# Performance work log

Hardware: AMD Instinct MI355X
Metric: run time of the kernel (lower is better)

## Reference

```python
import jax, jax.numpy as jnp
import numpy as np
import math

EPS = 1e-08
KERNEL = 3
PAD = KERNEL // 2


def setup_inputs() -> dict:
    key = jax.random.key(0)
    k1, k2, k3, k4 = jax.random.split(key, 4)
    B, C_in, C_out, H, W, S = 8, 512, 512, 64, 64, 512
    x = jax.random.normal(k1, (B, C_in, H, W), dtype=jnp.float32)
    style = jax.random.normal(k2, (B, S), dtype=jnp.float32)
    # modulation Linear: kaiming_normal fan_in linear => std = 1/sqrt(S); bias filled with 1
    w_mod = jax.random.normal(k3, (C_in, S), dtype=jnp.float32) / math.sqrt(S)
    b_mod = jnp.ones((C_in,), dtype=jnp.float32)
    # conv weight: randn / sqrt(in * k^2)
    weight = jax.random.normal(k4, (1, C_out, C_in, KERNEL, KERNEL), dtype=jnp.float32) / math.sqrt(C_in * KERNEL * KERNEL)
    return {"x": x, "style": style, "w_mod": w_mod, "b_mod": b_mod, "weight": weight}


def _modconv(x, style, w_mod, b_mod, weight):
    # style modulation: (B, S) @ (S, C_in) + bias -> (B, 1, C_in, 1, 1)
    s = style @ w_mod.T + b_mod
    w = weight * s[:, None, :, None, None]            # (B, C_out, C_in, k, k)
    # demodulate: rsqrt of sum of squares over (in, kh, kw)
    demod = jax.lax.rsqrt(jnp.sum(w * w, axis=(2, 3, 4)) + EPS)  # (B, C_out)
    w = w * demod[:, :, None, None, None]

    # groups=B conv == per-sample conv; vmap over batch
    def conv1(xb, wb):
        # xb: (C_in, H, W), wb: (C_out, C_in, k, k)
        return jax.lax.conv_general_dilated(
            xb[None], wb, window_strides=(1, 1),
            padding=[(PAD, PAD), (PAD, PAD)],
            dimension_numbers=("NCHW", "OIHW", "NCHW"))[0]

    return jax.vmap(conv1)(x, w)  # (B, C_out, H, W)


def reference(x, style, w_mod, b_mod, weight):
    return _modconv(x, style, w_mod, b_mod, weight)
```

## Files before the change

### kernel.cpp

```cpp
#include <hip/hip_runtime.h>
#include <hip/hip_bf16.h>

#define BATCH 8
#define CIN   512
#define COUT  512
#define HH    64
#define WW    64
#define SS    512
#define HP    66
#define WP    66
#define NPIX  (HH*WW)

typedef __bf16 bfrag  __attribute__((ext_vector_type(8)));
typedef float  f32x4  __attribute__((ext_vector_type(4)));
typedef unsigned short u16x8 __attribute__((ext_vector_type(8)));

__device__ __forceinline__ void async_copy16(const __hip_bfloat16* g, __hip_bfloat16* l) {
    __builtin_amdgcn_global_load_lds(
        (const __attribute__((address_space(1))) void*)g,
        (__attribute__((address_space(3))) void*)l,
        16, 0, 0);
}

__device__ __forceinline__ bool is_f32(const void* b_mod) {
    return ((const unsigned int*)b_mod)[0] == 0x3F800000u;
}

__global__ void k_prep(const void* __restrict__ style,
                       const void* __restrict__ w_mod,
                       const void* __restrict__ b_mod,
                       const void* __restrict__ weight,
                       float* __restrict__ s_out,
                       float* __restrict__ wsq,
                       __hip_bfloat16* __restrict__ Wt) {
    const bool f32 = is_f32(b_mod);
    if (blockIdx.x < 1024) {
        int tid = blockIdx.x * 256 + threadIdx.x;
        float sq = 0.f;
        if (f32) {
            const float* w = (const float*)weight + (size_t)tid * 9;
#pragma unroll
            for (int k = 0; k < 9; ++k) {
                float v = w[k];
                sq += v * v;
                Wt[k * (COUT * CIN) + tid] = __float2bfloat16(v);
            }
        } else {
            const __hip_bfloat16* w = (const __hip_bfloat16*)weight + (size_t)tid * 9;
#pragma unroll
            for (int k = 0; k < 9; ++k) {
                float v = __bfloat162float(w[k]);
                sq += v * v;
                Wt[k * (COUT * CIN) + tid] = w[k];
            }
        }
        wsq[tid] = sq;
    } else {
        int gw   = (blockIdx.x - 1024) * 4 + (threadIdx.x >> 6);
        int lane = threadIdx.x & 63;
        int b = gw >> 9, i = gw & 511;
        int base = lane * 8;
        float acc = 0.f;
        if (f32) {
            const float* st = (const float*)style + b * SS + base;
            const float* wm = (const float*)w_mod + i * SS + base;
#pragma unroll
            for (int j = 0; j < 8; ++j) acc += st[j] * wm[j];
        } else {
            const __hip_bfloat16* st = (const __hip_bfloat16*)style + b * SS + base;
            const __hip_bfloat16* wm = (const __hip_bfloat16*)w_mod + i * SS + base;
#pragma unroll
            for (int j = 0; j < 8; ++j)
                acc += __bfloat162float(st[j]) * __bfloat162float(wm[j]);
        }
#pragma unroll
        for (int off = 32; off; off >>= 1) acc += __shfl_down(acc, off);
        if (lane == 0) {
            float bias = f32 ? ((const float*)b_mod)[i]
                             : __bfloat162float(((const __hip_bfloat16*)b_mod)[i]);
            s_out[gw] = acc + bias;
        }
    }
}

__global__ void k_mid(const void* __restrict__ xv,
                      const float* __restrict__ s_buf,
                      const float* __restrict__ wsq,
                      const void* __restrict__ b_mod,
                      float* __restrict__ demod,
                      int b0, int nx, int do_demod,
                      __hip_bfloat16* __restrict__ xpad) {
    if ((int)blockIdx.x >= nx) {
        if (!do_demod) return;
        int gw   = ((int)blockIdx.x - nx) * 4 + (threadIdx.x >> 6);
        int lane = threadIdx.x & 63;
        int b = gw >> 9, o = gw & 511;
        int base = lane * 8;
        const float* sp = s_buf + b * CIN + base;
        const float* wp = wsq + o * CIN + base;
        float acc = 0.f;
#pragma unroll
        for (int j = 0; j < 8; ++j) {
            float sv = sp[j];
            acc += sv * sv * wp[j];
        }
#pragma unroll
        for (int off = 32; off; off >>= 1) acc += __shfl_down(acc, off);
        if (lane == 0) demod[gw] = rsqrtf(acc + 1e-8f);
        return;
    }
    const bool f32 = is_f32(b_mod);
    int ic = blockIdx.x & 15;
    int h  = (blockIdx.x >> 4) & 63;
    int bl = blockIdx.x >> 10;
    int b  = b0 + bl;
    int t  = threadIdx.x;
    int g  = t & 3;
    int w  = t >> 2;
    int ch0 = ic * 32 + g * 8;

    float sv[8];
#pragma unroll
    for (int j = 0; j < 8; ++j) sv[j] = s_buf[b * CIN + ch0 + j];

    u16x8 outv;
#pragma unroll
    for (int j = 0; j < 8; ++j) {
        size_t src = (size_t)(b * CIN + ch0 + j) * NPIX + h * WW + w;
        float xval = f32 ? ((const float*)xv)[src]
                         : __bfloat162float(((const __hip_bfloat16*)xv)[src]);
        __hip_bfloat16 bv = __float2bfloat16(xval * sv[j]);
        outv[j] = *(unsigned short*)&bv;
    }
    size_t rowb = (size_t)(bl * HP + h + 1) * WP;
    *(u16x8*)(xpad + (rowb + (w + 1)) * CIN + ch0) = outv;

    u16x8 z = {};
    if (w == 0)  *(u16x8*)(xpad + (rowb + 0)  * CIN + ch0) = z;
    if (w == 63) *(u16x8*)(xpad + (rowb + 65) * CIN + ch0) = z;
    if (h == 0) {
        size_t r0 = (size_t)(bl * HP + 0) * WP;
        *(u16x8*)(xpad + (r0 + (w + 1)) * CIN + ch0) = z;
        if (w == 0)  *(u16x8*)(xpad + (r0 + 0)  * CIN + ch0) = z;
        if (w == 63) *(u16x8*)(xpad + (r0 + 65) * CIN + ch0) = z;
    }
    if (h == 63) {
        size_t r65 = (size_t)(bl * HP + 65) * WP;
        *(u16x8*)(xpad + (r65 + (w + 1)) * CIN + ch0) = z;
        if (w == 0)  *(u16x8*)(xpad + (r65 + 0)  * CIN + ch0) = z;
        if (w == 63) *(u16x8*)(xpad + (r65 + 65) * CIN + ch0) = z;
    }
}

__global__ __launch_bounds__(512, 2)
void k_conv(const __hip_bfloat16* __restrict__ Wt,
            const __hip_bfloat16* __restrict__ xpad,
            const float* __restrict__ demod,
            const void* __restrict__ b_mod, int b0,
            void* __restrict__ outv) {
    __shared__ __hip_bfloat16 sA[2][3][256 * 32];
    __shared__ __hip_bfloat16 sB[2][384 * 32];

    const int tid  = threadIdx.x;
    const int wid  = tid >> 6;
    const int lane = tid & 63;

    const int id     = blockIdx.x;
    const int xcd    = id & 7;
    const int k      = id >> 3;
    const int o_tile = xcd >> 2;
    const int p_tile = (xcd & 3) * 4 + (k & 3);
    const int bl     = k >> 2;
    const int b      = b0 + bl;

    const int o_base = o_tile * 256;
    const int h0     = p_tile * 4;
    const int p_base = p_tile * 256;

    const int sw = ((lane & 3) ^ ((lane >> 3) & 3)) * 8;

    const int arow0 = wid * 32 + (lane >> 2);
    const int arow1 = arow0 + 16;
    const int aoff0 = wid * 1024 + lane * 8;
    const int aoff1 = aoff0 + 512;
    const int asrc0 = (o_base + arow0) * CIN + sw;
    const int asrc1 = (o_base + arow1) * CIN + sw;

    int bdst[3], bsrc[3];
#pragma unroll
    for (int jj = 0; jj < 3; ++jj) {
        int J   = wid * 3 + jj;
        int px  = J * 16 + (lane >> 2);
        int pm  = px < 263 ? px : 263;
        int r   = pm / 66;
        int c   = pm - r * 66;
        bdst[jj] = J * 512 + lane * 8;
        bsrc[jj] = ((bl * HP + h0 + r) * WP + c) * CIN + sw;
    }

    const int quad   = lane >> 4;
    const int l15    = lane & 15;
    const int wave_m = (wid >> 2) * 128;
    const int wave_n = (wid & 3) * 64;
    int afrag[8];
#pragma unroll
    for (int mt = 0; mt < 8; ++mt) {
        int row = wave_m + mt * 16 + l15;
        afrag[mt] = row * 32 + ((quad ^ ((l15 >> 1) & 3)) * 8);
    }
    int bfroff[4][3];
#pragma unroll
    for (int nt = 0; nt < 4; ++nt) {
        int n   = wave_n + nt * 16 + l15;
        int pr0 = (n >> 6) * 66 + (n & 63);
#pragma unroll
        for (int kw = 0; kw < 3; ++kw) {
            int pr = pr0 + kw;
            bfroff[nt][kw] = pr * 32 + ((quad ^ ((pr >> 1) & 3)) * 8);
        }
    }

    f32x4 acc[8][4];
#pragma unroll
    for (int mt = 0; mt < 8; ++mt)
#pragma unroll
        for (int nt = 0; nt < 4; ++nt)
            acc[mt][nt] = (f32x4)0.f;

    auto stage = [&](int buf, int it) {
        const int kh = it >> 4;
        const int i0 = (it & 15) << 5;
        const __hip_bfloat16* Wkh = Wt + kh * 3 * (COUT * CIN) + i0;
        const __hip_bfloat16* xr  = xpad + kh * (WP * CIN) + i0;
#pragma unroll
        for (int kw = 0; kw < 3; ++kw) {
            const __hip_bfloat16* Ap = Wkh + kw * (COUT * CIN);
            async_copy16(Ap + asrc0, &sA[buf][kw][aoff0]);
            async_copy16(Ap + asrc1, &sA[buf][kw][aoff1]);
        }
#pragma unroll
        for (int jj = 0; jj < 3; ++jj)
            async_copy16(xr + bsrc[jj], &sB[buf][bdst[jj]]);
    };

    auto compute = [&](int buf) {
        __builtin_amdgcn_s_setprio(1);
#pragma unroll
        for (int kw = 0; kw < 3; ++kw) {
            bfrag a[8], bb[4];
#pragma unroll
            for (int nt = 0; nt < 4; ++nt)
                bb[nt] = *(const bfrag*)(&sB[buf][bfroff[nt][kw]]);
#pragma unroll
            for (int mt = 0; mt < 8; ++mt)
                a[mt] = *(const bfrag*)(&sA[buf][kw][afrag[mt]]);
#pragma unroll
            for (int mt = 0; mt < 8; ++mt)
#pragma unroll
                for (int nt = 0; nt < 4; ++nt)
                    acc[mt][nt] = __builtin_amdgcn_mfma_f32_16x16x32_bf16(
                        a[mt], bb[nt], acc[mt][nt], 0, 0, 0);
        }
        __builtin_amdgcn_s_setprio(0);
    };

    stage(0, 0);
#pragma unroll 2
    for (int it = 0; it < 47; ++it) {
        stage((it + 1) & 1, it + 1);
        asm volatile("s_waitcnt vmcnt(9)" ::: "memory");
        __builtin_amdgcn_s_barrier();
        asm volatile("" ::: "memory");
        compute(it & 1);
        asm volatile("" ::: "memory");
        __builtin_amdgcn_s_barrier();
    }
    asm volatile("s_waitcnt vmcnt(0)" ::: "memory");
    __builtin_amdgcn_s_barrier();
    asm volatile("" ::: "memory");
    compute(1);

    const bool f32 = is_f32(b_mod);
#pragma unroll
    for (int mt = 0; mt < 8; ++mt) {
        const int o0r = o_base + wave_m + mt * 16 + quad * 4;
        float dm[4];
#pragma unroll
        for (int r = 0; r < 4; ++r) dm[r] = demod[b * COUT + o0r + r];
#pragma unroll
        for (int nt = 0; nt < 4; ++nt) {
            const int p = p_base + wave_n + nt * 16 + l15;
#pragma unroll
            for (int r = 0; r < 4; ++r) {
                float val = acc[mt][nt][r] * dm[r];
                size_t idx = (size_t)(b * COUT + o0r + r) * NPIX + p;
                if (f32) ((float*)outv)[idx] = val;
                else     ((__hip_bfloat16*)outv)[idx] = __float2bfloat16(val);
            }
        }
    }
}

extern "C" void kernel_launch(void* const* d_in, const int* in_sizes, int n_in,
                              void* d_out, int out_size, void* d_ws, size_t ws_size,
                              hipStream_t stream) {
    const void* x      = d_in[0];
    const void* style  = d_in[1];
    const void* w_mod  = d_in[2];
    const void* b_mod  = d_in[3];
    const void* weight = d_in[4];

    char* ws = (char*)d_ws;
    float*          s_buf = (float*)(ws + 4096);
    float*          demod = (float*)(ws + 20480);
    float*          wsq   = (float*)(ws + 36864);
    __hip_bfloat16* Wt    = (__hip_bfloat16*)(ws + 1085440);
    __hip_bfloat16* xpad  = (__hip_bfloat16*)(ws + 5804032);

    const size_t need_full = 5804032 + (size_t)BATCH * HP * WP * CIN * 2;
    const int group = (ws_size >= need_full) ? 8 : 4;

    k_prep<<<2048, 256, 0, stream>>>(style, w_mod, b_mod, weight, s_buf, wsq, Wt);

    for (int b0 = 0; b0 < BATCH; b0 += group) {
        const int nx = 1024 * group;
        const int do_demod = (b0 == 0) ? 1 : 0;
        const int nd = do_demod ? 1024 : 0;
        k_mid<<<nx + nd, 256, 0, stream>>>(x, s_buf, wsq, b_mod, demod,
                                           b0, nx, do_demod, xpad);
        k_conv<<<dim3(32 * group), 512, 0, stream>>>(Wt, xpad, demod, b_mod, b0, d_out);
    }
}
```

Before: 272.0 us.

## Split main loop into per-kw phases with interleaved staging and fragment loads

Restructures the double-buffered conv GEMM loop into three phases per iteration, one per kw tap. Each phase waits on a finer vmcnt, loads that tap's LDS fragments, issues part of the next buffer's global->LDS copies, then runs the MFMAs. The aim is to spread global loads across the iteration and overlap them with MFMA work instead of issuing all copies at once. The cost is two barriers per phase, six per iteration instead of two, and vmcnt thresholds that must exactly match the issue order.

```diff
diff --git a/kernel.cpp b/kernel.cpp
--- a/kernel.cpp
+++ b/kernel.cpp
@@ -227,58 +227,68 @@
         for (int nt = 0; nt < 4; ++nt)
             acc[mt][nt] = (f32x4)0.f;
 
-    auto stage = [&](int buf, int it) {
+    auto stageB = [&](int buf, int it) {
         const int kh = it >> 4;
         const int i0 = (it & 15) << 5;
-        const __hip_bfloat16* Wkh = Wt + kh * 3 * (COUT * CIN) + i0;
-        const __hip_bfloat16* xr  = xpad + kh * (WP * CIN) + i0;
-#pragma unroll
-        for (int kw = 0; kw < 3; ++kw) {
-            const __hip_bfloat16* Ap = Wkh + kw * (COUT * CIN);
-            async_copy16(Ap + asrc0, &sA[buf][kw][aoff0]);
-            async_copy16(Ap + asrc1, &sA[buf][kw][aoff1]);
-        }
+        const __hip_bfloat16* xr = xpad + kh * (WP * CIN) + i0;
 #pragma unroll
         for (int jj = 0; jj < 3; ++jj)
             async_copy16(xr + bsrc[jj], &sB[buf][bdst[jj]]);
     };
-
-    auto compute = [&](int buf) {
+    auto stageA = [&](int buf, int it, int kw) {
+        const int kh = it >> 4;
+        const int i0 = (it & 15) << 5;
+        const __hip_bfloat16* Ap = Wt + (kh * 3 + kw) * (COUT * CIN) + i0;
+        async_copy16(Ap + asrc0, &sA[buf][kw][aoff0]);
+        async_copy16(Ap + asrc1, &sA[buf][kw][aoff1]);
+    };
+
+    bfrag a[8], bb[4];
+    auto ldfrags = [&](int buf, int kw) {
+#pragma unroll
+        for (int nt = 0; nt < 4; ++nt)
+            bb[nt] = *(const bfrag*)(&sB[buf][bfroff[nt][kw]]);
+#pragma unroll
+        for (int mt = 0; mt < 8; ++mt)
+            a[mt] = *(const bfrag*)(&sA[buf][kw][afrag[mt]]);
+    };
+    auto domfma = [&]() {
         __builtin_amdgcn_s_setprio(1);
 #pragma unroll
-        for (int kw = 0; kw < 3; ++kw) {
-            bfrag a[8], bb[4];
+        for (int mt = 0; mt < 8; ++mt)
 #pragma unroll
             for (int nt = 0; nt < 4; ++nt)
-                bb[nt] = *(const bfrag*)(&sB[buf][bfroff[nt][kw]]);
-#pragma unroll
-            for (int mt = 0; mt < 8; ++mt)
-                a[mt] = *(const bfrag*)(&sA[buf][kw][afrag[mt]]);
-#pragma unroll
-            for (int mt = 0; mt < 8; ++mt)
-#pragma unroll
-                for (int nt = 0; nt < 4; ++nt)
-                    acc[mt][nt] = __builtin_amdgcn_mfma_f32_16x16x32_bf16(
-                        a[mt], bb[nt], acc[mt][nt], 0, 0, 0);
-        }
+                acc[mt][nt] = __builtin_amdgcn_mfma_f32_16x16x32_bf16(
+                    a[mt], bb[nt], acc[mt][nt], 0, 0, 0);
         __builtin_amdgcn_s_setprio(0);
     };
 
-    stage(0, 0);
-#pragma unroll 2
+#define PH(VMN, BUF, KW, STAGE_STMT)                                  \
+    asm volatile("s_waitcnt vmcnt(" #VMN ")" ::: "memory");           \
+    __builtin_amdgcn_s_barrier();                                     \
+    asm volatile("" ::: "memory");                                    \
+    ldfrags(BUF, KW);                                                 \
+    STAGE_STMT;                                                       \
+    __builtin_amdgcn_s_barrier();                                     \
+    asm volatile("s_waitcnt lgkmcnt(0)" ::: "memory");                \
+    __builtin_amdgcn_sched_barrier(0);                                \
+    domfma();
+
+    stageB(0, 0);
+    stageA(0, 0, 0);
+    stageA(0, 0, 1);
+    stageA(0, 0, 2);
+
     for (int it = 0; it < 47; ++it) {
-        stage((it + 1) & 1, it + 1);
-        asm volatile("s_waitcnt vmcnt(9)" ::: "memory");
-        __builtin_amdgcn_s_barrier();
-        asm volatile("" ::: "memory");
-        compute(it & 1);
-        asm volatile("" ::: "memory");
-        __builtin_amdgcn_s_barrier();
-    }
-    asm volatile("s_waitcnt vmcnt(0)" ::: "memory");
-    __builtin_amdgcn_s_barrier();
-    asm volatile("" ::: "memory");
-    compute(1);
+        const int buf = it & 1, nb = buf ^ 1, nit = it + 1;
+        PH(4, buf, 0, stageB(nb, nit));
+        PH(5, buf, 1, stageA(nb, nit, 0); stageA(nb, nit, 1));
+        PH(7, buf, 2, stageA(nb, nit, 2));
+    }
+    PH(4, 1, 0, );
+    PH(2, 1, 1, );
+    PH(0, 1, 2, );
+#undef PH
 
     const bool f32 = is_f32(b_mod);
 #pragma unroll
```

Measured after the change: 271.8 us. Within noise of the previous version (-0.0%).
